# Performance work log

Measured on AMD Instinct MI355X. Metric: run time of the kernel, lower is better.

Reference implementation:

```python
import jax, jax.numpy as jnp
import numpy as np

N = 100000
E = 1600000
EPS = 1e-5  # BatchNorm eps


def setup_inputs() -> dict:
    key = jax.random.key(0)
    ks = jax.random.split(key, 8)
    x = jax.random.normal(ks[0], (N, 8), jnp.float32)
    edge_index = jax.random.randint(ks[1], (2, E), 0, N, dtype=jnp.int64)

    def lin(k, i, o):
        return jax.random.normal(k, (i, o), jnp.float32) / np.float32(np.sqrt(i))

    d = {
        'x': x, 'edge_index': edge_index,
        'W1': lin(ks[2], 8, 64),  'b1': jnp.zeros((64,), jnp.float32),
        'g1': jnp.ones((64,), jnp.float32), 'be1': jnp.zeros((64,), jnp.float32),
        'rm1': jnp.zeros((64,), jnp.float32), 'rv1': jnp.ones((64,), jnp.float32),
        'W2': lin(ks[3], 64, 64), 'b2': jnp.zeros((64,), jnp.float32),
        'g2': jnp.ones((64,), jnp.float32), 'be2': jnp.zeros((64,), jnp.float32),
        'rm2': jnp.zeros((64,), jnp.float32), 'rv2': jnp.ones((64,), jnp.float32),
        'W3': lin(ks[4], 64, 32), 'b3': jnp.zeros((32,), jnp.float32),
        'g3': jnp.ones((32,), jnp.float32), 'be3': jnp.zeros((32,), jnp.float32),
        'rm3': jnp.zeros((32,), jnp.float32), 'rv3': jnp.ones((32,), jnp.float32),
        'Wc': lin(ks[5], 32, 2),  'bc': jnp.zeros((2,), jnp.float32),
    }
    return d


def _gcn_conv(x, W, b, src, dst):
    # PyG GCNConv (improved=False): add self-loops with weight 1, symmetric norm.
    h = x @ W                                               # [N, out]
    deg = jax.ops.segment_sum(jnp.ones((E,), x.dtype), dst, num_segments=N) + 1.0
    dinv = jax.lax.rsqrt(deg)                               # deg >= 1 (self loop)
    norm = dinv[src] * dinv[dst]                            # [E]
    agg = jax.ops.segment_sum(h[src] * norm[:, None], dst, num_segments=N)
    agg = agg + h * (dinv * dinv)[:, None]                  # self-loop messages
    return agg + b


def _bn_eval(x, g, be, rm, rv):
    return (x - rm) * jax.lax.rsqrt(rv + EPS) * g + be


def reference(x, edge_index,
              W1, b1, g1, be1, rm1, rv1,
              W2, b2, g2, be2, rm2, rv2,
              W3, b3, g3, be3, rm3, rv3,
              Wc, bc):
    src, dst = edge_index[0], edge_index[1]
    h = jax.nn.relu(_bn_eval(_gcn_conv(x, W1, b1, src, dst), g1, be1, rm1, rv1))
    h = jax.nn.relu(_bn_eval(_gcn_conv(h, W2, b2, src, dst), g2, be2, rm2, rv2))
    h = jax.nn.relu(_bn_eval(_gcn_conv(h, W3, b3, src, dst), g3, be3, rm3, rv3))
    logits = h @ Wc + bc                                    # [N, 2]
    return jax.nn.log_softmax(logits, axis=-1)
```

## Files before the change

### kernel.cpp

```cpp
#include <hip/hip_runtime.h>
#include <hip/hip_fp16.h>

#define BN_EPS 1e-5f
#define BCAP 5120
#define EDCAP_H64 768
#define EDCAP_CLS 1280

__device__ __forceinline__ unsigned f2u(float a, float b) {
  __half2 h = __floats2half2_rn(a, b);
  return *reinterpret_cast<unsigned*>(&h);
}
__device__ __forceinline__ __half2 uh2(unsigned u) {
  return *reinterpret_cast<__half2*>(&u);
}
__device__ __forceinline__ float2 h22f2(__half2 h) { return __half22float2(h); }
__device__ __forceinline__ __half2 h2shfl_xor(__half2 v, int m) {
  int i = *reinterpret_cast<int*>(&v);
  i = __shfl_xor(i, m);
  return *reinterpret_cast<__half2*>(&i);
}

__global__ void prep(const float* __restrict__ b1, const float* __restrict__ g1,
                     const float* __restrict__ be1, const float* __restrict__ rm1,
                     const float* __restrict__ rv1,
                     const float* __restrict__ b2, const float* __restrict__ g2,
                     const float* __restrict__ be2, const float* __restrict__ rm2,
                     const float* __restrict__ rv2,
                     const float* __restrict__ b3, const float* __restrict__ g3,
                     const float* __restrict__ be3, const float* __restrict__ rm3,
                     const float* __restrict__ rv3,
                     float* __restrict__ bn, int* __restrict__ bcur, int NB) {
  if (blockIdx.x == 0) {
    const int t = threadIdx.x;
    if (t < 64) {
      const float s = g1[t] * rsqrtf(rv1[t] + BN_EPS);
      bn[t] = s;
      bn[64 + t] = (b1[t] - rm1[t]) * s + be1[t];
    } else if (t < 128) {
      const int c = t - 64;
      const float s = g2[c] * rsqrtf(rv2[c] + BN_EPS);
      bn[128 + c] = s;
      bn[192 + c] = (b2[c] - rm2[c]) * s + be2[c];
    } else if (t < 160) {
      const int c = t - 128;
      const float s = g3[c] * rsqrtf(rv3[c] + BN_EPS);
      bn[256 + c] = s;
      bn[288 + c] = (b3[c] - rm3[c]) * s + be3[c];
    }
  } else {
    const int i = (blockIdx.x - 1) * 256 + threadIdx.x;
    if (i <= NB) bcur[i] = 0;
  }
}

__global__ void p1_partition(const int* __restrict__ ei, int* __restrict__ bucketbuf,
                             int* __restrict__ bcur, int E_, int NB) {
  __shared__ int pk[4096];
  __shared__ short bk[4096];
  __shared__ int hist[512];
  __shared__ int bbase[512];
  const int tid = threadIdx.x;
  const int e0 = blockIdx.x * 4096;
  const int ecount = min(4096, E_ - e0);
  for (int i = tid; i < NB; i += 256) hist[i] = 0;
  __syncthreads();
  for (int i = tid; i < ecount; i += 256) {
    const int s = ei[e0 + i];
    const int d = ei[(size_t)E_ + e0 + i];
    pk[i] = ((d & 255) << 24) | s;
    const int b = d >> 8;
    bk[i] = (short)b;
    atomicAdd(&hist[b], 1);
  }
  __syncthreads();
  for (int i = tid; i < NB; i += 256) {
    const int c = hist[i];
    bbase[i] = c ? atomicAdd(&bcur[i], c) : 0;
    hist[i] = 0;
  }
  __syncthreads();
  for (int i = tid; i < ecount; i += 256) {
    const int b = bk[i];
    const int slot = bbase[b] + atomicAdd(&hist[b], 1);
    bucketbuf[(size_t)b * BCAP + slot] = pk[i];
  }
}

__global__ void p2_sort(const int* __restrict__ bucketbuf, const int* __restrict__ bcur,
                        int* __restrict__ gcursor, int* __restrict__ edata,
                        int* __restrict__ rbeg, int* __restrict__ rend,
                        float* __restrict__ dinv, const float* __restrict__ x,
                        __half2* __restrict__ xs, int N_) {
  __shared__ int cntl[256];
  __shared__ int scn[256];
  __shared__ int cur[256];
  __shared__ float dinvl[256];
  __shared__ int sbuf[BCAP];
  __shared__ int sbase;
  const int b = blockIdx.x;
  const int tid = threadIdx.x;
  const int m = bcur[b];
  const int* srcp = bucketbuf + (size_t)b * BCAP;
  cntl[tid] = 0;
  __syncthreads();
  for (int i = tid; i < m; i += 256) atomicAdd(&cntl[(unsigned)srcp[i] >> 24], 1);
  __syncthreads();
  if (tid == 0) sbase = atomicAdd(gcursor, m);
  const int cnt = cntl[tid];
  scn[tid] = cnt;
  __syncthreads();
  for (int off = 1; off < 256; off <<= 1) {
    int u = (tid >= off) ? scn[tid - off] : 0;
    __syncthreads();
    scn[tid] += u;
    __syncthreads();
  }
  const int excl = scn[tid] - cnt;
  cur[tid] = excl;
  const int base = sbase;
  const int node = (b << 8) + tid;
  const float dn = rsqrtf((float)cnt + 1.0f);
  dinvl[tid] = dn;
  if (node < N_) {
    rbeg[node] = base + excl;
    rend[node] = base + excl + cnt;
    dinv[node] = dn;
  }
  __syncthreads();
  for (int i = tid; i < m; i += 256) {
    const int v = srcp[i];
    const int slot = atomicAdd(&cur[(unsigned)v >> 24], 1);
    sbuf[slot] = v & 0xFFFFFF;
  }
  __syncthreads();
  for (int i = tid; i < m; i += 256) edata[(size_t)base + i] = sbuf[i];
  const int nb0 = b << 8;
  for (int i = tid; i < 1024; i += 256) {
    const int nd = nb0 + (i >> 2);
    if (nd < N_) {
      const float d2 = dinvl[i >> 2];
      const float2 v2 = reinterpret_cast<const float2*>(x)[(size_t)nd * 4 + (i & 3)];
      xs[(size_t)nd * 4 + (i & 3)] = __floats2half2_rn(v2.x * d2, v2.y * d2);
    }
  }
}

__global__ void l12(const __half* __restrict__ xs, const float* __restrict__ dinv,
                    const int* __restrict__ rbeg, const int* __restrict__ rend,
                    const int* __restrict__ edata, const float* __restrict__ W1,
                    const float* __restrict__ W2, const float* __restrict__ bn,
                    __half* __restrict__ h2, int n) {
  __shared__ float shw1[8 * 64];
  __shared__ float shagg[32][8];
  __shared__ __half2 sht1[32 * 33];
  __shared__ uint4 shw2[32 * 16];
  const int tid = threadIdx.x;
  const int node0 = blockIdx.x * 32;
  for (int i = tid; i < 512; i += 256) shw1[i] = W1[i];
  {
    __half2* shw2h = reinterpret_cast<__half2*>(shw2);
    for (int i = tid; i < 32 * 64; i += 256) {
      const int kp = i >> 6, c = i & 63;
      shw2h[kp * 64 + c] = __floats2half2_rn(W2[(2 * kp) * 64 + c], W2[(2 * kp + 1) * 64 + c]);
    }
  }
  const int lane = tid & 63;
  const int nl = ((tid >> 6) << 3) + (lane >> 3);
  const int grp = lane & 7;
  const int node = node0 + nl;
  if (node < n) {
    const int beg = rbeg[node], end = rend[node];
    const uint4* xv = reinterpret_cast<const uint4*>(xs);
    __half2 c0 = __half2{0, 0}, c1 = c0, c2 = c0, c3 = c0;
    int e = beg + grp;
    for (; e + 8 < end; e += 16) {
      const uint4 q0 = xv[edata[e]];
      const uint4 q1 = xv[edata[e + 8]];
      c0 = __hadd2(c0, uh2(q0.x)); c1 = __hadd2(c1, uh2(q0.y));
      c2 = __hadd2(c2, uh2(q0.z)); c3 = __hadd2(c3, uh2(q0.w));
      c0 = __hadd2(c0, uh2(q1.x)); c1 = __hadd2(c1, uh2(q1.y));
      c2 = __hadd2(c2, uh2(q1.z)); c3 = __hadd2(c3, uh2(q1.w));
    }
    if (e < end) {
      const uint4 q = xv[edata[e]];
      c0 = __hadd2(c0, uh2(q.x)); c1 = __hadd2(c1, uh2(q.y));
      c2 = __hadd2(c2, uh2(q.z)); c3 = __hadd2(c3, uh2(q.w));
    }
#pragma unroll
    for (int m = 1; m <= 4; m <<= 1) {
      c0 = __hadd2(c0, h2shfl_xor(c0, m));
      c1 = __hadd2(c1, h2shfl_xor(c1, m));
      c2 = __hadd2(c2, h2shfl_xor(c2, m));
      c3 = __hadd2(c3, h2shfl_xor(c3, m));
    }
    if (grp == 0) {
      const uint4 q = xv[node];
      c0 = __hadd2(c0, uh2(q.x)); c1 = __hadd2(c1, uh2(q.y));
      c2 = __hadd2(c2, uh2(q.z)); c3 = __hadd2(c3, uh2(q.w));
      const float dn = dinv[node];
      const float2 f0 = h22f2(c0), f1 = h22f2(c1);
      const float2 f2 = h22f2(c2), f3 = h22f2(c3);
      shagg[nl][0] = f0.x * dn; shagg[nl][1] = f0.y * dn;
      shagg[nl][2] = f1.x * dn; shagg[nl][3] = f1.y * dn;
      shagg[nl][4] = f2.x * dn; shagg[nl][5] = f2.y * dn;
      shagg[nl][6] = f3.x * dn; shagg[nl][7] = f3.y * dn;
    }
  }
  __syncthreads();
  {
    const int mn = tid >> 3;
    const int c = (tid & 7) * 8;
    if (node0 + mn < n) {
      float a[8] = {0, 0, 0, 0, 0, 0, 0, 0};
#pragma unroll
      for (int k = 0; k < 8; ++k) {
        const float s = shagg[mn][k];
#pragma unroll
        for (int j = 0; j < 8; ++j) a[j] += s * shw1[k * 64 + c + j];
      }
      float v[8];
#pragma unroll
      for (int j = 0; j < 8; ++j) {
        float t = a[j] * bn[c + j] + bn[64 + c + j];
        v[j] = t > 0.0f ? t : 0.0f;
      }
#pragma unroll
      for (int j = 0; j < 4; ++j)
        sht1[mn * 33 + (tid & 7) * 4 + j] = __floats2half2_rn(v[2 * j], v[2 * j + 1]);
    }
  }
  __syncthreads();
  const int cq = tid & 15;
  const int nbs = (tid >> 4) * 2;
  float acc[2][4];
#pragma unroll
  for (int j = 0; j < 2; ++j)
#pragma unroll
    for (int k = 0; k < 4; ++k) acc[j][k] = 0.0f;
  for (int kp = 0; kp < 32; ++kp) {
    const uint4 wq = shw2[kp * 16 + cq];
    const float2 w0 = h22f2(uh2(wq.x)), w1 = h22f2(uh2(wq.y));
    const float2 w2 = h22f2(uh2(wq.z)), w3 = h22f2(uh2(wq.w));
#pragma unroll
    for (int j = 0; j < 2; ++j) {
      const float2 s = h22f2(sht1[(nbs + j) * 33 + kp]);
      acc[j][0] += s.x * w0.x + s.y * w0.y;
      acc[j][1] += s.x * w1.x + s.y * w1.y;
      acc[j][2] += s.x * w2.x + s.y * w2.y;
      acc[j][3] += s.x * w3.x + s.y * w3.y;
    }
  }
#pragma unroll
  for (int j = 0; j < 2; ++j) {
    const int nd = node0 + nbs + j;
    if (nd < n) {
      const float dn = dinv[nd];
      uint2 o;
      o.x = f2u(acc[j][0] * dn, acc[j][1] * dn);
      o.y = f2u(acc[j][2] * dn, acc[j][3] * dn);
      reinterpret_cast<uint2*>(h2)[(size_t)nd * 16 + cq] = o;
    }
  }
}

__global__ void gh64_mm3(const __half* __restrict__ h, const float* __restrict__ dinv,
                         const int* __restrict__ rbeg, const int* __restrict__ rend,
                         const int* __restrict__ edata, const float* __restrict__ W3,
                         const float* __restrict__ bn, __half* __restrict__ h3, int n) {
  __shared__ int se[EDCAP_H64];
  __shared__ __half2 shagg2[8 * 33];
  __shared__ __half2 shw3[32 * 32];
  __shared__ float shbn[128];
  const int tid = threadIdx.x;
  const int node0 = blockIdx.x * 8;
  const int last = min(node0 + 7, n - 1);
  const int gb = rbeg[node0];
  const int total = rend[last] - gb;
  const bool lds = (total <= EDCAP_H64);
  if (lds) {
    for (int i = tid; i < total; i += 256) se[i] = edata[gb + i];
  }
  for (int i = tid; i < 32 * 32; i += 256) {
    const int kp = i >> 5, c = i & 31;
    shw3[kp * 32 + c] = __floats2half2_rn(W3[(2 * kp) * 32 + c], W3[(2 * kp + 1) * 32 + c]);
  }
  if (tid < 128) shbn[tid] = bn[128 + tid];
  __syncthreads();
  const int lane = tid & 63;
  const int node = node0 + ((tid >> 6) << 1) + (lane >> 5);
  const int sub = lane & 31;
  const int qi = sub & 7;
  const int grp = sub >> 3;
  if (node < n) {
    const uint4* hv = reinterpret_cast<const uint4*>(h);
    __half2 c0 = __half2{0, 0}, c1 = c0, c2 = c0, c3 = c0;
    if (lds) {
      const int beg = rbeg[node] - gb, end = rend[node] - gb;
      int e = beg + grp;
      for (; e + 12 < end; e += 16) {
        const int s0 = se[e], s1 = se[e + 4], s2 = se[e + 8], s3 = se[e + 12];
        const uint4 q0 = hv[(size_t)s0 * 8 + qi];
        const uint4 q1 = hv[(size_t)s1 * 8 + qi];
        const uint4 q2 = hv[(size_t)s2 * 8 + qi];
        const uint4 q3 = hv[(size_t)s3 * 8 + qi];
        c0 = __hadd2(c0, uh2(q0.x)); c1 = __hadd2(c1, uh2(q0.y));
        c2 = __hadd2(c2, uh2(q0.z)); c3 = __hadd2(c3, uh2(q0.w));
        c0 = __hadd2(c0, uh2(q1.x)); c1 = __hadd2(c1, uh2(q1.y));
        c2 = __hadd2(c2, uh2(q1.z)); c3 = __hadd2(c3, uh2(q1.w));
        c0 = __hadd2(c0, uh2(q2.x)); c1 = __hadd2(c1, uh2(q2.y));
        c2 = __hadd2(c2, uh2(q2.z)); c3 = __hadd2(c3, uh2(q2.w));
        c0 = __hadd2(c0, uh2(q3.x)); c1 = __hadd2(c1, uh2(q3.y));
        c2 = __hadd2(c2, uh2(q3.z)); c3 = __hadd2(c3, uh2(q3.w));
      }
      for (; e < end; e += 4) {
        const uint4 q = hv[(size_t)se[e] * 8 + qi];
        c0 = __hadd2(c0, uh2(q.x)); c1 = __hadd2(c1, uh2(q.y));
        c2 = __hadd2(c2, uh2(q.z)); c3 = __hadd2(c3, uh2(q.w));
      }
    } else {
      const int beg = rbeg[node], end = rend[node];
      int e = beg + grp;
      for (; e + 12 < end; e += 16) {
        const int s0 = edata[e], s1 = edata[e + 4], s2 = edata[e + 8], s3 = edata[e + 12];
        const uint4 q0 = hv[(size_t)s0 * 8 + qi];
        const uint4 q1 = hv[(size_t)s1 * 8 + qi];
        const uint4 q2 = hv[(size_t)s2 * 8 + qi];
        const uint4 q3 = hv[(size_t)s3 * 8 + qi];
        c0 = __hadd2(c0, uh2(q0.x)); c1 = __hadd2(c1, uh2(q0.y));
        c2 = __hadd2(c2, uh2(q0.z)); c3 = __hadd2(c3, uh2(q0.w));
        c0 = __hadd2(c0, uh2(q1.x)); c1 = __hadd2(c1, uh2(q1.y));
        c2 = __hadd2(c2, uh2(q1.z)); c3 = __hadd2(c3, uh2(q1.w));
        c0 = __hadd2(c0, uh2(q2.x)); c1 = __hadd2(c1, uh2(q2.y));
        c2 = __hadd2(c2, uh2(q2.z)); c3 = __hadd2(c3, uh2(q2.w));
        c0 = __hadd2(c0, uh2(q3.x)); c1 = __hadd2(c1, uh2(q3.y));
        c2 = __hadd2(c2, uh2(q3.z)); c3 = __hadd2(c3, uh2(q3.w));
      }
      for (; e < end; e += 4) {
        const uint4 q = hv[(size_t)edata[e] * 8 + qi];
        c0 = __hadd2(c0, uh2(q.x)); c1 = __hadd2(c1, uh2(q.y));
        c2 = __hadd2(c2, uh2(q.z)); c3 = __hadd2(c3, uh2(q.w));
      }
    }
#pragma unroll
    for (int m = 8; m <= 16; m <<= 1) {
      c0 = __hadd2(c0, h2shfl_xor(c0, m));
      c1 = __hadd2(c1, h2shfl_xor(c1, m));
      c2 = __hadd2(c2, h2shfl_xor(c2, m));
      c3 = __hadd2(c3, h2shfl_xor(c3, m));
    }
    if (grp == 0) {
      const uint4 q = hv[(size_t)node * 8 + qi];
      c0 = __hadd2(c0, uh2(q.x)); c1 = __hadd2(c1, uh2(q.y));
      c2 = __hadd2(c2, uh2(q.z)); c3 = __hadd2(c3, uh2(q.w));
      const float dn = dinv[node];
      const int nl = node - node0;
      const float2 f[4] = {h22f2(c0), h22f2(c1), h22f2(c2), h22f2(c3)};
#pragma unroll
      for (int j = 0; j < 4; ++j) {
        const int ch = qi * 8 + 2 * j;
        float v0 = f[j].x * dn * shbn[ch] + shbn[64 + ch];
        float v1 = f[j].y * dn * shbn[ch + 1] + shbn[64 + ch + 1];
        v0 = v0 > 0.0f ? v0 : 0.0f;
        v1 = v1 > 0.0f ? v1 : 0.0f;
        shagg2[nl * 33 + qi * 4 + j] = __floats2half2_rn(v0, v1);
      }
    }
  }
  __syncthreads();
  const int mnode = node0 + (tid >> 5);
  const int c = tid & 31;
  float acc = 0.0f;
#pragma unroll 8
  for (int kp = 0; kp < 32; ++kp) {
    const float2 s = h22f2(shagg2[(tid >> 5) * 33 + kp]);
    const float2 w = h22f2(shw3[kp * 32 + c]);
    acc += s.x * w.x + s.y * w.y;
  }
  float outv = 0.0f;
  if (mnode < n) outv = acc * dinv[mnode];
  const float partner = __shfl_xor(outv, 1);
  if ((c & 1) == 0 && mnode < n) {
    reinterpret_cast<unsigned*>(h3)[(size_t)mnode * 16 + (c >> 1)] = f2u(outv, partner);
  }
}

__global__ void gather_cls(const __half* __restrict__ h, const float* __restrict__ dinv,
                           const int* __restrict__ rbeg, const int* __restrict__ rend,
                           const int* __restrict__ edata, const float* __restrict__ bn,
                           const float* __restrict__ Wc, const float* __restrict__ bc,
                           float* __restrict__ out, int n) {
  __shared__ int se[EDCAP_CLS];
  const int tid = threadIdx.x;
  const int node0 = blockIdx.x * 16;
  const int last = min(node0 + 15, n - 1);
  const int gb = rbeg[node0];
  const int total = rend[last] - gb;
  const bool lds = (total <= EDCAP_CLS);
  if (lds) {
    for (int i = tid; i < total; i += 256) se[i] = edata[gb + i];
  }
  __syncthreads();
  const int lane = tid & 63;
  const int node = node0 + ((tid >> 6) << 2) + (lane >> 4);
  if (node >= n) return;
  const int qi = lane & 3;
  const int grp = (lane >> 2) & 3;
  const uint4* hv = reinterpret_cast<const uint4*>(h);
  __half2 c0 = __half2{0, 0}, c1 = c0, c2 = c0, c3 = c0;
  if (lds) {
    const int beg = rbeg[node] - gb, end = rend[node] - gb;
    int e = beg + grp;
    for (; e + 12 < end; e += 16) {
      const int s0 = se[e], s1 = se[e + 4], s2 = se[e + 8], s3 = se[e + 12];
      const uint4 q0 = hv[(size_t)s0 * 4 + qi];
      const uint4 q1 = hv[(size_t)s1 * 4 + qi];
      const uint4 q2 = hv[(size_t)s2 * 4 + qi];
      const uint4 q3 = hv[(size_t)s3 * 4 + qi];
      c0 = __hadd2(c0, uh2(q0.x)); c1 = __hadd2(c1, uh2(q0.y));
      c2 = __hadd2(c2, uh2(q0.z)); c3 = __hadd2(c3, uh2(q0.w));
      c0 = __hadd2(c0, uh2(q1.x)); c1 = __hadd2(c1, uh2(q1.y));
      c2 = __hadd2(c2, uh2(q1.z)); c3 = __hadd2(c3, uh2(q1.w));
      c0 = __hadd2(c0, uh2(q2.x)); c1 = __hadd2(c1, uh2(q2.y));
      c2 = __hadd2(c2, uh2(q2.z)); c3 = __hadd2(c3, uh2(q2.w));
      c0 = __hadd2(c0, uh2(q3.x)); c1 = __hadd2(c1, uh2(q3.y));
      c2 = __hadd2(c2, uh2(q3.z)); c3 = __hadd2(c3, uh2(q3.w));
    }
    for (; e < end; e += 4) {
      const uint4 q = hv[(size_t)se[e] * 4 + qi];
      c0 = __hadd2(c0, uh2(q.x)); c1 = __hadd2(c1, uh2(q.y));
      c2 = __hadd2(c2, uh2(q.z)); c3 = __hadd2(c3, uh2(q.w));
    }
  } else {
    const int beg = rbeg[node], end = rend[node];
    int e = beg + grp;
    for (; e + 12 < end; e += 16) {
      const int s0 = edata[e], s1 = edata[e + 4], s2 = edata[e + 8], s3 = edata[e + 12];
      const uint4 q0 = hv[(size_t)s0 * 4 + qi];
      const uint4 q1 = hv[(size_t)s1 * 4 + qi];
      const uint4 q2 = hv[(size_t)s2 * 4 + qi];
      const uint4 q3 = hv[(size_t)s3 * 4 + qi];
      c0 = __hadd2(c0, uh2(q0.x)); c1 = __hadd2(c1, uh2(q0.y));
      c2 = __hadd2(c2, uh2(q0.z)); c3 = __hadd2(c3, uh2(q0.w));
      c0 = __hadd2(c0, uh2(q1.x)); c1 = __hadd2(c1, uh2(q1.y));
      c2 = __hadd2(c2, uh2(q1.z)); c3 = __hadd2(c3, uh2(q1.w));
      c0 = __hadd2(c0, uh2(q2.x)); c1 = __hadd2(c1, uh2(q2.y));
      c2 = __hadd2(c2, uh2(q2.z)); c3 = __hadd2(c3, uh2(q2.w));
      c0 = __hadd2(c0, uh2(q3.x)); c1 = __hadd2(c1, uh2(q3.y));
      c2 = __hadd2(c2, uh2(q3.z)); c3 = __hadd2(c3, uh2(q3.w));
    }
    for (; e < end; e += 4) {
      const uint4 q = hv[(size_t)edata[e] * 4 + qi];
      c0 = __hadd2(c0, uh2(q.x)); c1 = __hadd2(c1, uh2(q.y));
      c2 = __hadd2(c2, uh2(q.z)); c3 = __hadd2(c3, uh2(q.w));
    }
  }
#pragma unroll
  for (int m = 4; m <= 8; m <<= 1) {
    c0 = __hadd2(c0, h2shfl_xor(c0, m));
    c1 = __hadd2(c1, h2shfl_xor(c1, m));
    c2 = __hadd2(c2, h2shfl_xor(c2, m));
    c3 = __hadd2(c3, h2shfl_xor(c3, m));
  }
  if (grp != 0) return;
  {
    const uint4 q = hv[(size_t)node * 4 + qi];
    c0 = __hadd2(c0, uh2(q.x)); c1 = __hadd2(c1, uh2(q.y));
    c2 = __hadd2(c2, uh2(q.z)); c3 = __hadd2(c3, uh2(q.w));
  }
  const float dn = dinv[node];
  const float2 f0 = h22f2(c0), f1 = h22f2(c1);
  const float2 f2 = h22f2(c2), f3 = h22f2(c3);
  const float v[8] = {f0.x * dn, f0.y * dn, f1.x * dn, f1.y * dn,
                      f2.x * dn, f2.y * dn, f3.x * dn, f3.y * dn};
  float l0 = 0.0f, l1 = 0.0f;
#pragma unroll
  for (int j = 0; j < 8; ++j) {
    const int c = qi * 8 + j;
    float t = v[j] * bn[256 + c] + bn[288 + c];
    t = t > 0.0f ? t : 0.0f;
    const float2 w = *reinterpret_cast<const float2*>(&Wc[c * 2]);
    l0 += t * w.x;
    l1 += t * w.y;
  }
  l0 += __shfl_xor(l0, 1); l1 += __shfl_xor(l1, 1);
  l0 += __shfl_xor(l0, 2); l1 += __shfl_xor(l1, 2);
  if (qi == 0) {
    l0 += bc[0];
    l1 += bc[1];
    const float m = fmaxf(l0, l1);
    const float lse = m + log1pf(expf(-fabsf(l0 - l1)));
    *reinterpret_cast<float2*>(&out[(size_t)node * 2]) = make_float2(l0 - lse, l1 - lse);
  }
}

extern "C" void kernel_launch(void* const* d_in, const int* in_sizes, int n_in,
                              void* d_out, int out_size, void* d_ws, size_t ws_size,
                              hipStream_t stream) {
  const float* x  = (const float*)d_in[0];
  const int* ei   = (const int*)d_in[1];
  const float* W1 = (const float*)d_in[2];
  const float* b1 = (const float*)d_in[3];
  const float* g1 = (const float*)d_in[4];
  const float* be1 = (const float*)d_in[5];
  const float* rm1 = (const float*)d_in[6];
  const float* rv1 = (const float*)d_in[7];
  const float* W2 = (const float*)d_in[8];
  const float* b2 = (const float*)d_in[9];
  const float* g2 = (const float*)d_in[10];
  const float* be2 = (const float*)d_in[11];
  const float* rm2 = (const float*)d_in[12];
  const float* rv2 = (const float*)d_in[13];
  const float* W3 = (const float*)d_in[14];
  const float* b3 = (const float*)d_in[15];
  const float* g3 = (const float*)d_in[16];
  const float* be3 = (const float*)d_in[17];
  const float* rm3 = (const float*)d_in[18];
  const float* rv3 = (const float*)d_in[19];
  const float* Wc = (const float*)d_in[20];
  const float* bc = (const float*)d_in[21];

  const int N_ = in_sizes[0] / 8;
  const int E_ = in_sizes[1] / 2;
  const int NB = (N_ + 255) >> 8;

  auto align = [](size_t v) { return (v + 255) & ~(size_t)255; };
  char* ws = (char*)d_ws;
  size_t off = 0;
  float* dinv   = (float*)(ws + off); off += align((size_t)N_ * 4);
  int* bcur     = (int*)(ws + off);   off += align(((size_t)NB + 1) * 4);
  int* rbeg     = (int*)(ws + off);   off += align((size_t)N_ * 4);
  int* rend     = (int*)(ws + off);   off += align((size_t)N_ * 4);
  float* bnbuf  = (float*)(ws + off); off += align(320 * 4);
  int* edata    = (int*)(ws + off);   off += align((size_t)E_ * 4);
  __half* xs    = (__half*)(ws + off); off += align((size_t)N_ * 8 * 2);
  char* regionA = ws + off;           off += align((size_t)NB * BCAP * 4);
  char* regionB = ws + off;           off += align((size_t)N_ * 64 * 2);

  int* bucketbuf = (int*)regionA;
  __half* h3   = (__half*)regionA;
  __half* h2   = (__half*)regionB;
  int* gcursor = bcur + NB;

  prep<<<1 + (NB + 1 + 255) / 256, 256, 0, stream>>>(b1, g1, be1, rm1, rv1,
                                                     b2, g2, be2, rm2, rv2,
                                                     b3, g3, be3, rm3, rv3, bnbuf, bcur, NB);
  p1_partition<<<(E_ + 4095) / 4096, 256, 0, stream>>>(ei, bucketbuf, bcur, E_, NB);
  p2_sort<<<NB, 256, 0, stream>>>(bucketbuf, bcur, gcursor, edata, rbeg, rend,
                                  dinv, x, (__half2*)xs, N_);

  l12<<<(N_ + 31) / 32, 256, 0, stream>>>(xs, dinv, rbeg, rend, edata, W1, W2, bnbuf, h2, N_);

  gh64_mm3<<<(N_ + 7) / 8, 256, 0, stream>>>(h2, dinv, rbeg, rend, edata, W3, bnbuf, h3, N_);

  gather_cls<<<(N_ + 15) / 16, 256, 0, stream>>>(h3, dinv, rbeg, rend, edata,
                                                 bnbuf, Wc, bc, (float*)d_out, N_);
}
```

Baseline: 156.3 us.

## Stage neighbor feature rows into LDS and halve nodes per block in gathers

In the layer-3 gather and classifier gather kernels, each block now first copies all neighbor feature rows for its nodes into shared memory, with flat coalesced slot assignment across the block, and then reduces from LDS. Nodes per block are halved and each node gets a full wave (or half wave) with 8 edge groups instead of 4. The goal is to spread the irregular gathers more evenly across threads and expose more loads in flight. In exchange, the BN scale and shift are read from global memory instead of LDS, and half the threads sit idle in the small matmul. Blocks whose edges exceed the small staging capacity fall back to an un-unrolled direct gather.

Result: slower. 187.1 us (+19.8%).

```diff
diff --git a/kernel.cpp b/kernel.cpp
--- a/kernel.cpp
+++ b/kernel.cpp
@@ -3,8 +3,8 @@
 
 #define BN_EPS 1e-5f
 #define BCAP 5120
-#define EDCAP_H64 768
-#define EDCAP_CLS 1280
+#define STG_H 96
+#define STG_C 160
 
 __device__ __forceinline__ unsigned f2u(float a, float b) {
   __half2 h = __floats2half2_rn(a, b);
@@ -267,82 +267,56 @@
                          const int* __restrict__ rbeg, const int* __restrict__ rend,
                          const int* __restrict__ edata, const float* __restrict__ W3,
                          const float* __restrict__ bn, __half* __restrict__ h3, int n) {
-  __shared__ int se[EDCAP_H64];
-  __shared__ __half2 shagg2[8 * 33];
+  __shared__ int se[STG_H];
+  __shared__ uint4 sstage[STG_H * 8];
+  __shared__ __half2 shagg2[4 * 33];
   __shared__ __half2 shw3[32 * 32];
-  __shared__ float shbn[128];
   const int tid = threadIdx.x;
-  const int node0 = blockIdx.x * 8;
-  const int last = min(node0 + 7, n - 1);
+  const int node0 = blockIdx.x * 4;
+  const int last = min(node0 + 3, n - 1);
   const int gb = rbeg[node0];
   const int total = rend[last] - gb;
-  const bool lds = (total <= EDCAP_H64);
-  if (lds) {
-    for (int i = tid; i < total; i += 256) se[i] = edata[gb + i];
-  }
+  const bool lds = (total <= STG_H);
   for (int i = tid; i < 32 * 32; i += 256) {
     const int kp = i >> 5, c = i & 31;
     shw3[kp * 32 + c] = __floats2half2_rn(W3[(2 * kp) * 32 + c], W3[(2 * kp + 1) * 32 + c]);
   }
-  if (tid < 128) shbn[tid] = bn[128 + tid];
+  const uint4* hv = reinterpret_cast<const uint4*>(h);
+  if (lds) {
+    for (int i = tid; i < total; i += 256) se[i] = edata[gb + i];
+  }
+  __syncthreads();
+  if (lds) {
+    const int nslots = total * 8;
+    for (int slot = tid; slot < nslots; slot += 256) {
+      const int e = slot >> 3, q = slot & 7;
+      sstage[slot] = hv[(size_t)se[e] * 8 + q];
+    }
+  }
   __syncthreads();
   const int lane = tid & 63;
-  const int node = node0 + ((tid >> 6) << 1) + (lane >> 5);
-  const int sub = lane & 31;
-  const int qi = sub & 7;
-  const int grp = sub >> 3;
+  const int node = node0 + (tid >> 6);
+  const int qi = lane & 7;
+  const int grp = lane >> 3;
   if (node < n) {
-    const uint4* hv = reinterpret_cast<const uint4*>(h);
     __half2 c0 = __half2{0, 0}, c1 = c0, c2 = c0, c3 = c0;
     if (lds) {
-      const int beg = rbeg[node] - gb, end = rend[node] - gb;
-      int e = beg + grp;
-      for (; e + 12 < end; e += 16) {
-        const int s0 = se[e], s1 = se[e + 4], s2 = se[e + 8], s3 = se[e + 12];
-        const uint4 q0 = hv[(size_t)s0 * 8 + qi];
-        const uint4 q1 = hv[(size_t)s1 * 8 + qi];
-        const uint4 q2 = hv[(size_t)s2 * 8 + qi];
-        const uint4 q3 = hv[(size_t)s3 * 8 + qi];
-        c0 = __hadd2(c0, uh2(q0.x)); c1 = __hadd2(c1, uh2(q0.y));
-        c2 = __hadd2(c2, uh2(q0.z)); c3 = __hadd2(c3, uh2(q0.w));
-        c0 = __hadd2(c0, uh2(q1.x)); c1 = __hadd2(c1, uh2(q1.y));
-        c2 = __hadd2(c2, uh2(q1.z)); c3 = __hadd2(c3, uh2(q1.w));
-        c0 = __hadd2(c0, uh2(q2.x)); c1 = __hadd2(c1, uh2(q2.y));
-        c2 = __hadd2(c2, uh2(q2.z)); c3 = __hadd2(c3, uh2(q2.w));
-        c0 = __hadd2(c0, uh2(q3.x)); c1 = __hadd2(c1, uh2(q3.y));
-        c2 = __hadd2(c2, uh2(q3.z)); c3 = __hadd2(c3, uh2(q3.w));
-      }
-      for (; e < end; e += 4) {
-        const uint4 q = hv[(size_t)se[e] * 8 + qi];
+      const int lbeg = rbeg[node] - gb, lend = rend[node] - gb;
+      for (int e = lbeg + grp; e < lend; e += 8) {
+        const uint4 q = sstage[e * 8 + qi];
         c0 = __hadd2(c0, uh2(q.x)); c1 = __hadd2(c1, uh2(q.y));
         c2 = __hadd2(c2, uh2(q.z)); c3 = __hadd2(c3, uh2(q.w));
       }
     } else {
       const int beg = rbeg[node], end = rend[node];
-      int e = beg + grp;
-      for (; e + 12 < end; e += 16) {
-        const int s0 = edata[e], s1 = edata[e + 4], s2 = edata[e + 8], s3 = edata[e + 12];
-        const uint4 q0 = hv[(size_t)s0 * 8 + qi];
-        const uint4 q1 = hv[(size_t)s1 * 8 + qi];
-        const uint4 q2 = hv[(size_t)s2 * 8 + qi];
-        const uint4 q3 = hv[(size_t)s3 * 8 + qi];
-        c0 = __hadd2(c0, uh2(q0.x)); c1 = __hadd2(c1, uh2(q0.y));
-        c2 = __hadd2(c2, uh2(q0.z)); c3 = __hadd2(c3, uh2(q0.w));
-        c0 = __hadd2(c0, uh2(q1.x)); c1 = __hadd2(c1, uh2(q1.y));
-        c2 = __hadd2(c2, uh2(q1.z)); c3 = __hadd2(c3, uh2(q1.w));
-        c0 = __hadd2(c0, uh2(q2.x)); c1 = __hadd2(c1, uh2(q2.y));
-        c2 = __hadd2(c2, uh2(q2.z)); c3 = __hadd2(c3, uh2(q2.w));
-        c0 = __hadd2(c0, uh2(q3.x)); c1 = __hadd2(c1, uh2(q3.y));
-        c2 = __hadd2(c2, uh2(q3.z)); c3 = __hadd2(c3, uh2(q3.w));
-      }
-      for (; e < end; e += 4) {
+      for (int e = beg + grp; e < end; e += 8) {
         const uint4 q = hv[(size_t)edata[e] * 8 + qi];
         c0 = __hadd2(c0, uh2(q.x)); c1 = __hadd2(c1, uh2(q.y));
         c2 = __hadd2(c2, uh2(q.z)); c3 = __hadd2(c3, uh2(q.w));
       }
     }
 #pragma unroll
-    for (int m = 8; m <= 16; m <<= 1) {
+    for (int m = 8; m <= 32; m <<= 1) {
       c0 = __hadd2(c0, h2shfl_xor(c0, m));
       c1 = __hadd2(c1, h2shfl_xor(c1, m));
       c2 = __hadd2(c2, h2shfl_xor(c2, m));
@@ -358,8 +332,8 @@
 #pragma unroll
       for (int j = 0; j < 4; ++j) {
         const int ch = qi * 8 + 2 * j;
-        float v0 = f[j].x * dn * shbn[ch] + shbn[64 + ch];
-        float v1 = f[j].y * dn * shbn[ch + 1] + shbn[64 + ch + 1];
+        float v0 = f[j].x * dn * bn[128 + ch] + bn[192 + ch];
+        float v1 = f[j].y * dn * bn[128 + ch + 1] + bn[192 + ch + 1];
         v0 = v0 > 0.0f ? v0 : 0.0f;
         v1 = v1 > 0.0f ? v1 : 0.0f;
         shagg2[nl * 33 + qi * 4 + j] = __floats2half2_rn(v0, v1);
@@ -367,20 +341,22 @@
     }
   }
   __syncthreads();
-  const int mnode = node0 + (tid >> 5);
-  const int c = tid & 31;
-  float acc = 0.0f;
+  if (tid < 128) {
+    const int mnode = node0 + (tid >> 5);
+    const int c = tid & 31;
+    float acc = 0.0f;
 #pragma unroll 8
-  for (int kp = 0; kp < 32; ++kp) {
-    const float2 s = h22f2(shagg2[(tid >> 5) * 33 + kp]);
-    const float2 w = h22f2(shw3[kp * 32 + c]);
-    acc += s.x * w.x + s.y * w.y;
-  }
-  float outv = 0.0f;
-  if (mnode < n) outv = acc * dinv[mnode];
-  const float partner = __shfl_xor(outv, 1);
-  if ((c & 1) == 0 && mnode < n) {
-    reinterpret_cast<unsigned*>(h3)[(size_t)mnode * 16 + (c >> 1)] = f2u(outv, partner);
+    for (int kp = 0; kp < 32; ++kp) {
+      const float2 s = h22f2(shagg2[(tid >> 5) * 33 + kp]);
+      const float2 w = h22f2(shw3[kp * 32 + c]);
+      acc += s.x * w.x + s.y * w.y;
+    }
+    float outv = 0.0f;
+    if (mnode < n) outv = acc * dinv[mnode];
+    const float partner = __shfl_xor(outv, 1);
+    if ((c & 1) == 0 && mnode < n) {
+      reinterpret_cast<unsigned*>(h3)[(size_t)mnode * 16 + (c >> 1)] = f2u(outv, partner);
+    }
   }
 }
 
@@ -389,73 +365,51 @@
                            const int* __restrict__ edata, const float* __restrict__ bn,
                            const float* __restrict__ Wc, const float* __restrict__ bc,
                            float* __restrict__ out, int n) {
-  __shared__ int se[EDCAP_CLS];
+  __shared__ int se[STG_C];
+  __shared__ uint4 sstage[STG_C * 4];
   const int tid = threadIdx.x;
-  const int node0 = blockIdx.x * 16;
-  const int last = min(node0 + 15, n - 1);
+  const int node0 = blockIdx.x * 8;
+  const int last = min(node0 + 7, n - 1);
   const int gb = rbeg[node0];
   const int total = rend[last] - gb;
-  const bool lds = (total <= EDCAP_CLS);
+  const bool lds = (total <= STG_C);
+  const uint4* hv = reinterpret_cast<const uint4*>(h);
   if (lds) {
     for (int i = tid; i < total; i += 256) se[i] = edata[gb + i];
   }
   __syncthreads();
+  if (lds) {
+    const int nslots = total * 4;
+    for (int slot = tid; slot < nslots; slot += 256) {
+      const int e = slot >> 2, q = slot & 3;
+      sstage[slot] = hv[(size_t)se[e] * 4 + q];
+    }
+  }
+  __syncthreads();
   const int lane = tid & 63;
-  const int node = node0 + ((tid >> 6) << 2) + (lane >> 4);
+  const int node = node0 + ((tid >> 6) << 1) + (lane >> 5);
   if (node >= n) return;
-  const int qi = lane & 3;
-  const int grp = (lane >> 2) & 3;
-  const uint4* hv = reinterpret_cast<const uint4*>(h);
+  const int sub = lane & 31;
+  const int qi = sub & 3;
+  const int grp = sub >> 2;
   __half2 c0 = __half2{0, 0}, c1 = c0, c2 = c0, c3 = c0;
   if (lds) {
-    const int beg = rbeg[node] - gb, end = rend[node] - gb;
-    int e = beg + grp;
-    for (; e + 12 < end; e += 16) {
-      const int s0 = se[e], s1 = se[e + 4], s2 = se[e + 8], s3 = se[e + 12];
-      const uint4 q0 = hv[(size_t)s0 * 4 + qi];
-      const uint4 q1 = hv[(size_t)s1 * 4 + qi];
-      const uint4 q2 = hv[(size_t)s2 * 4 + qi];
-      const uint4 q3 = hv[(size_t)s3 * 4 + qi];
-      c0 = __hadd2(c0, uh2(q0.x)); c1 = __hadd2(c1, uh2(q0.y));
-      c2 = __hadd2(c2, uh2(q0.z)); c3 = __hadd2(c3, uh2(q0.w));
-      c0 = __hadd2(c0, uh2(q1.x)); c1 = __hadd2(c1, uh2(q1.y));
-      c2 = __hadd2(c2, uh2(q1.z)); c3 = __hadd2(c3, uh2(q1.w));
-      c0 = __hadd2(c0, uh2(q2.x)); c1 = __hadd2(c1, uh2(q2.y));
-      c2 = __hadd2(c2, uh2(q2.z)); c3 = __hadd2(c3, uh2(q2.w));
-      c0 = __hadd2(c0, uh2(q3.x)); c1 = __hadd2(c1, uh2(q3.y));
-      c2 = __hadd2(c2, uh2(q3.z)); c3 = __hadd2(c3, uh2(q3.w));
-    }
-    for (; e < end; e += 4) {
-      const uint4 q = hv[(size_t)se[e] * 4 + qi];
+    const int lbeg = rbeg[node] - gb, lend = rend[node] - gb;
+    for (int e = lbeg + grp; e < lend; e += 8) {
+      const uint4 q = sstage[e * 4 + qi];
       c0 = __hadd2(c0, uh2(q.x)); c1 = __hadd2(c1, uh2(q.y));
       c2 = __hadd2(c2, uh2(q.z)); c3 = __hadd2(c3, uh2(q.w));
     }
   } else {
     const int beg = rbeg[node], end = rend[node];
-    int e = beg + grp;
-    for (; e + 12 < end; e += 16) {
-      const int s0 = edata[e], s1 = edata[e + 4], s2 = edata[e + 8], s3 = edata[e + 12];
-      const uint4 q0 = hv[(size_t)s0 * 4 + qi];
-      const uint4 q1 = hv[(size_t)s1 * 4 + qi];
-      const uint4 q2 = hv[(size_t)s2 * 4 + qi];
-      const uint4 q3 = hv[(size_t)s3 * 4 + qi];
-      c0 = __hadd2(c0, uh2(q0.x)); c1 = __hadd2(c1, uh2(q0.y));
-      c2 = __hadd2(c2, uh2(q0.z)); c3 = __hadd2(c3, uh2(q0.w));
-      c0 = __hadd2(c0, uh2(q1.x)); c1 = __hadd2(c1, uh2(q1.y));
-      c2 = __hadd2(c2, uh2(q1.z)); c3 = __hadd2(c3, uh2(q1.w));
-      c0 = __hadd2(c0, uh2(q2.x)); c1 = __hadd2(c1, uh2(q2.y));
-      c2 = __hadd2(c2, uh2(q2.z)); c3 = __hadd2(c3, uh2(q2.w));
-      c0 = __hadd2(c0, uh2(q3.x)); c1 = __hadd2(c1, uh2(q3.y));
-      c2 = __hadd2(c2, uh2(q3.z)); c3 = __hadd2(c3, uh2(q3.w));
-    }
-    for (; e < end; e += 4) {
+    for (int e = beg + grp; e < end; e += 8) {
       const uint4 q = hv[(size_t)edata[e] * 4 + qi];
       c0 = __hadd2(c0, uh2(q.x)); c1 = __hadd2(c1, uh2(q.y));
       c2 = __hadd2(c2, uh2(q.z)); c3 = __hadd2(c3, uh2(q.w));
     }
   }
 #pragma unroll
-  for (int m = 4; m <= 8; m <<= 1) {
+  for (int m = 4; m <= 16; m <<= 1) {
     c0 = __hadd2(c0, h2shfl_xor(c0, m));
     c1 = __hadd2(c1, h2shfl_xor(c1, m));
     c2 = __hadd2(c2, h2shfl_xor(c2, m));
@@ -550,8 +504,8 @@
 
   l12<<<(N_ + 31) / 32, 256, 0, stream>>>(xs, dinv, rbeg, rend, edata, W1, W2, bnbuf, h2, N_);
 
-  gh64_mm3<<<(N_ + 7) / 8, 256, 0, stream>>>(h2, dinv, rbeg, rend, edata, W3, bnbuf, h3, N_);
-
-  gather_cls<<<(N_ + 15) / 16, 256, 0, stream>>>(h3, dinv, rbeg, rend, edata,
-                                                 bnbuf, Wc, bc, (float*)d_out, N_);
-}
+  gh64_mm3<<<(N_ + 3) / 4, 256, 0, stream>>>(h2, dinv, rbeg, rend, edata, W3, bnbuf, h3, N_);
+
+  gather_cls<<<(N_ + 7) / 8, 256, 0, stream>>>(h3, dinv, rbeg, rend, edata,
+                                               bnbuf, Wc, bc, (float*)d_out, N_);
+}
```
